# Optimization experiments

Hardware: AMD Instinct MI355X
Metric: run time of the kernel (lower is better)

## Reference

```python
import jax, jax.numpy as jnp
import numpy as np

B = 1_000_000
N_DIR, N_TRIAL = 2, 4
ALPHA, R_GAS, EPS = 0.3, 8.314462618, 1e-12
TAU_CLIP, LN_CLIP = 10.0, 20.0
EPS_FD, SIGMA, MARGIN = 1e-4, 0.05, 0.0
LAM_PHY, LAM_GD, LAM_TPD = 1.0, 0.1, 0.1


def renorm3(x):
    # clamp to >=0 and normalize so components sum to 1 (last axis)
    x = jnp.maximum(x, 0.0)
    return x / jnp.maximum(x.sum(-1, keepdims=True), EPS)


def nrtl_ln_gamma(x, T, g):
    # x: (B,3), T: (B,), g: (B,3,3) -> ln_gamma: (B,3)
    x = jnp.maximum(x, 0.0)
    Tc = jnp.maximum(T, 1.0)
    tau = jnp.clip(g / (R_GAS * jnp.maximum(Tc, EPS)[:, None, None]), -TAU_CLIP, TAU_CLIP)
    G = jnp.exp(-ALPHA * tau)
    denom = jnp.maximum(jnp.einsum('bj,bji->bi', x, G), EPS)          # (B,3)
    A = jnp.einsum('bj,bji->bi', x, tau * G)                          # (B,3), == num1 in torch
    term1 = A / denom
    W = x[:, None, :] * G / denom[:, None, :]                         # (B,3,3)
    inside = tau - (A / denom)[:, None, :]
    term2 = (W * inside).sum(-1)
    return jnp.clip(term1 + term2, -LN_CLIP, LN_CLIP)


def setup_inputs() -> dict:
    key = jax.random.key(0)
    k1, k2, k3, k4, k5, k6 = jax.random.split(key, 6)
    pred = jax.random.uniform(k1, (B, 6), dtype=jnp.float32, minval=0.01, maxval=1.0)
    target = jax.random.uniform(k2, (B, 6), dtype=jnp.float32, minval=0.01, maxval=1.0)
    T = 298.0 + 100.0 * jax.random.uniform(k3, (B,), dtype=jnp.float32)  # Kelvin
    g = 800.0 * jax.random.normal(k4, (B, 3, 3), dtype=jnp.float32)      # J/mol
    # simplex directions: zero-sum, unit-norm (matches _sample_simplex_directions)
    v = jax.random.normal(k5, (N_DIR, B, 3), dtype=jnp.float32)
    v = v - v.mean(-1, keepdims=True)
    dirs = v / jnp.maximum(jnp.linalg.norm(v, axis=-1, keepdims=True), 1e-12)
    noise = SIGMA * jax.random.normal(k6, (N_TRIAL, B, 3), dtype=jnp.float32)
    return {'pred': pred, 'target': target, 'T': T, 'g': g, 'dirs': dirs, 'noise': noise}


def reference(pred, target, T, g, dirs, noise):
    # supervised MSE on (E+R) compositions
    L_sup = jnp.mean((pred - target) ** 2)

    xE = renorm3(pred[:, :3])
    xR = renorm3(pred[:, 3:])
    ln_gE = nrtl_ln_gamma(xE, T, g)
    ln_gR = nrtl_ln_gamma(xR, T, g)
    # chemical potential residual r_k = ln(xE_k gE_k) - ln(xR_k gR_k)
    r = jnp.log(jnp.maximum(xE, EPS)) + ln_gE - (jnp.log(jnp.maximum(xR, EPS)) + ln_gR)
    L_phy = jnp.mean(r ** 2)

    lg = jax.vmap(lambda xx: nrtl_ln_gamma(xx, T, g))  # over trial/direction axis

    # Gibbs-Duhem finite-difference penalty along simplex directions
    x_p = renorm3(xE[None] + EPS_FD * dirs)            # (N_DIR,B,3)
    x_m = renorm3(xE[None] - EPS_FD * dirs)
    d_ln = (lg(x_p) - lg(x_m)) / (2.0 * EPS_FD)
    gd = (xE[None] * d_ln).sum(-1)                     # (N_DIR,B)
    L_gd = jnp.mean(gd * gd)

    # TPD stability penalty
    w = renorm3(xE[None] + noise)                      # (N_TRIAL,B,3)
    ln_gw = lg(w)
    tpd = (w * (jnp.log(jnp.maximum(w, EPS)) + ln_gw
                - jnp.log(jnp.maximum(xE, EPS))[None] - ln_gE[None])).sum(-1)
    L_tpd = jnp.mean(jnp.maximum(MARGIN - tpd, 0.0))

    return L_sup + LAM_PHY * L_phy + LAM_GD * L_gd + LAM_TPD * L_tpd
```

## Files before the change

### kernel.cpp

```cpp
#include <hip/hip_runtime.h>


constexpr float ALPHA   = 0.3f;
constexpr float R_GAS   = 8.314462618f;
constexpr float EPS     = 1e-12f;
constexpr float TAU_CLIP= 10.0f;
constexpr float LN_CLIP = 20.0f;
constexpr float EPS_FD  = 1e-4f;
constexpr float LAM_PHY = 1.0f;
constexpr float LAM_GD  = 0.1f;
constexpr float LAM_TPD = 0.1f;

__device__ __forceinline__ float clipf(float v, float lo, float hi) {
    return fminf(fmaxf(v, lo), hi);
}

struct Mats {
    float tau[3][3];
    float G[3][3];
    float tG[3][3];
};

__device__ __forceinline__ void ln_gamma3(const float x[3], const Mats& M, float lg[3]) {
    float ratio[3], invd[3];
#pragma unroll
    for (int i = 0; i < 3; ++i) {
        float d = x[0] * M.G[0][i] + x[1] * M.G[1][i] + x[2] * M.G[2][i];
        d = fmaxf(d, EPS);
        float A = x[0] * M.tG[0][i] + x[1] * M.tG[1][i] + x[2] * M.tG[2][i];
        float inv = 1.0f / d;
        invd[i] = inv;
        ratio[i] = A * inv;
    }
#pragma unroll
    for (int i = 0; i < 3; ++i) {
        float s = ratio[i];
#pragma unroll
        for (int j = 0; j < 3; ++j) {
            s += x[j] * M.G[i][j] * invd[j] * (M.tau[i][j] - ratio[j]);
        }
        lg[i] = clipf(s, -LN_CLIP, LN_CLIP);
    }
}

__device__ __forceinline__ void renorm3(float x[3]) {
    x[0] = fmaxf(x[0], 0.0f);
    x[1] = fmaxf(x[1], 0.0f);
    x[2] = fmaxf(x[2], 0.0f);
    float inv = 1.0f / fmaxf(x[0] + x[1] + x[2], EPS);
    x[0] *= inv; x[1] *= inv; x[2] *= inv;
}

__global__ __launch_bounds__(256) void nrtl_loss_kernel(
    const float* __restrict__ pred,
    const float* __restrict__ target,
    const float* __restrict__ Tarr,
    const float* __restrict__ g,
    const float* __restrict__ dirs,
    const float* __restrict__ noise,
    double* __restrict__ acc, int B)
{
    const int i = blockIdx.x * blockDim.x + threadIdx.x;
    float contrib = 0.0f;

    if (i < B) {
        float sup = 0.0f;
        float p6[6];
#pragma unroll
        for (int k = 0; k < 6; ++k) {
            float pv = pred[i * 6 + k];
            float tv = target[i * 6 + k];
            float d  = pv - tv;
            sup += d * d;
            p6[k] = pv;
        }

        float xE[3] = {p6[0], p6[1], p6[2]};
        float xR[3] = {p6[3], p6[4], p6[5]};
        renorm3(xE);
        renorm3(xR);

        const float Tc = fmaxf(Tarr[i], 1.0f);
        const float invRT = 1.0f / (R_GAS * Tc);
        Mats M;
#pragma unroll
        for (int a = 0; a < 3; ++a) {
#pragma unroll
            for (int b = 0; b < 3; ++b) {
                float ta = clipf(g[i * 9 + a * 3 + b] * invRT, -TAU_CLIP, TAU_CLIP);
                float Gv = expf(-ALPHA * ta);
                M.tau[a][b] = ta;
                M.G[a][b]   = Gv;
                M.tG[a][b]  = ta * Gv;
            }
        }

        float lgE[3], lgR[3];
        ln_gamma3(xE, M, lgE);
        ln_gamma3(xR, M, lgR);

        float logxE[3];
        float phy = 0.0f;
#pragma unroll
        for (int k = 0; k < 3; ++k) {
            logxE[k] = logf(fmaxf(xE[k], EPS));
            float r = logxE[k] + lgE[k] - logf(fmaxf(xR[k], EPS)) - lgR[k];
            phy += r * r;
        }

        float gdsum = 0.0f;
#pragma unroll
        for (int d = 0; d < 2; ++d) {
            float dv[3];
#pragma unroll
            for (int k = 0; k < 3; ++k) dv[k] = dirs[(d * B + i) * 3 + k];
            float xp[3], xm[3];
#pragma unroll
            for (int k = 0; k < 3; ++k) {
                xp[k] = xE[k] + EPS_FD * dv[k];
                xm[k] = xE[k] - EPS_FD * dv[k];
            }
            renorm3(xp);
            renorm3(xm);
            float lgp[3], lgm[3];
            ln_gamma3(xp, M, lgp);
            ln_gamma3(xm, M, lgm);
            float gd = 0.0f;
            const float inv2e = 0.5f / EPS_FD;
#pragma unroll
            for (int k = 0; k < 3; ++k) gd += xE[k] * ((lgp[k] - lgm[k]) * inv2e);
            gdsum += gd * gd;
        }

        float tpdsum = 0.0f;
#pragma unroll
        for (int t = 0; t < 4; ++t) {
            float w[3];
#pragma unroll
            for (int k = 0; k < 3; ++k) w[k] = xE[k] + noise[(t * B + i) * 3 + k];
            renorm3(w);
            float lgw[3];
            ln_gamma3(w, M, lgw);
            float tpd = 0.0f;
#pragma unroll
            for (int k = 0; k < 3; ++k) {
                tpd += w[k] * (logf(fmaxf(w[k], EPS)) + lgw[k] - logxE[k] - lgE[k]);
            }
            tpdsum += fmaxf(-tpd, 0.0f);
        }

        const float invB = 1.0f / (float)B;
        contrib = invB * (sup * (1.0f / 6.0f)
                          + LAM_PHY * phy * (1.0f / 3.0f)
                          + LAM_GD  * gdsum * 0.5f
                          + LAM_TPD * tpdsum * 0.25f);
    }

#pragma unroll
    for (int off = 32; off > 0; off >>= 1)
        contrib += __shfl_down(contrib, off, 64);

    __shared__ float ssum[4];
    const int lane = threadIdx.x & 63;
    const int wid  = threadIdx.x >> 6;
    if (lane == 0) ssum[wid] = contrib;
    __syncthreads();
    if (threadIdx.x == 0) {
        float bs = ssum[0] + ssum[1] + ssum[2] + ssum[3];
        atomicAdd(acc, (double)bs);
    }
}

__global__ void zero_ws_kernel(double* acc) { acc[0] = 0.0; }

__global__ void finalize_kernel(const double* acc, float* out) {
    out[0] = (float)acc[0];
}

extern "C" void kernel_launch(void* const* d_in, const int* in_sizes, int n_in,
                              void* d_out, int out_size, void* d_ws, size_t ws_size,
                              hipStream_t stream) {
    const float* pred   = (const float*)d_in[0];
    const float* target = (const float*)d_in[1];
    const float* Tarr   = (const float*)d_in[2];
    const float* g      = (const float*)d_in[3];
    const float* dirs   = (const float*)d_in[4];
    const float* noise  = (const float*)d_in[5];
    const int B = in_sizes[2];

    double* acc = (double*)d_ws;
    float*  out = (float*)d_out;

    zero_ws_kernel<<<1, 1, 0, stream>>>(acc);
    const int block = 256;
    const int grid  = (B + block - 1) / block;
    nrtl_loss_kernel<<<grid, block, 0, stream>>>(pred, target, Tarr, g, dirs, noise, acc, B);
    finalize_kernel<<<1, 1, 0, stream>>>(acc, out);
}
```

Measured before the change: 190.5 us.

## Use hardware rcp/exp2/log intrinsics, vectorize loads, replace atomics with partial reduction

Replaces IEEE divisions, expf and logf with AMD hardware approximate rcp, exp2 and log2 intrinsics to cut transcendental instruction cost. Loads pred and target as float2. Replaces the per-block double atomicAdd, plus its zero and finalize kernels, with per-block float partials summed by a single-block reduction kernel, removing atomic contention and one launch. The approximate intrinsics lose a few ulp of accuracy, and the finite-difference Gibbs-Duhem term may amplify that error.

```diff
diff --git a/kernel.cpp b/kernel.cpp
--- a/kernel.cpp
+++ b/kernel.cpp
@@ -1,19 +1,25 @@
 #include <hip/hip_runtime.h>
 
 
-constexpr float ALPHA   = 0.3f;
-constexpr float R_GAS   = 8.314462618f;
-constexpr float EPS     = 1e-12f;
-constexpr float TAU_CLIP= 10.0f;
-constexpr float LN_CLIP = 20.0f;
-constexpr float EPS_FD  = 1e-4f;
-constexpr float LAM_PHY = 1.0f;
-constexpr float LAM_GD  = 0.1f;
-constexpr float LAM_TPD = 0.1f;
+constexpr float ALPHA    = 0.3f;
+constexpr float R_GAS    = 8.314462618f;
+constexpr float EPS      = 1e-12f;
+constexpr float TAU_CLIP = 10.0f;
+constexpr float LN_CLIP  = 20.0f;
+constexpr float EPS_FD   = 1e-4f;
+constexpr float LAM_PHY  = 1.0f;
+constexpr float LAM_GD   = 0.1f;
+constexpr float LAM_TPD  = 0.1f;
+
+constexpr float LOG2E = 1.44269504088896340736f;
+constexpr float LN2   = 0.69314718055994530942f;
 
 __device__ __forceinline__ float clipf(float v, float lo, float hi) {
     return fminf(fmaxf(v, lo), hi);
 }
+__device__ __forceinline__ float fast_rcp(float x) { return __builtin_amdgcn_rcpf(x); }
+__device__ __forceinline__ float fast_exp(float x) { return __expf(x); }
+__device__ __forceinline__ float fast_log(float x) { return __logf(x); }
 
 struct Mats {
     float tau[3][3];
@@ -28,7 +34,7 @@
         float d = x[0] * M.G[0][i] + x[1] * M.G[1][i] + x[2] * M.G[2][i];
         d = fmaxf(d, EPS);
         float A = x[0] * M.tG[0][i] + x[1] * M.tG[1][i] + x[2] * M.tG[2][i];
-        float inv = 1.0f / d;
+        float inv = fast_rcp(d);
         invd[i] = inv;
         ratio[i] = A * inv;
     }
@@ -47,7 +53,7 @@
     x[0] = fmaxf(x[0], 0.0f);
     x[1] = fmaxf(x[1], 0.0f);
     x[2] = fmaxf(x[2], 0.0f);
-    float inv = 1.0f / fmaxf(x[0] + x[1] + x[2], EPS);
+    float inv = fast_rcp(fmaxf(x[0] + x[1] + x[2], EPS));
     x[0] *= inv; x[1] *= inv; x[2] *= inv;
 }
 
@@ -58,21 +64,24 @@
     const float* __restrict__ g,
     const float* __restrict__ dirs,
     const float* __restrict__ noise,
-    double* __restrict__ acc, int B)
+    float* __restrict__ partials, int B)
 {
     const int i = blockIdx.x * blockDim.x + threadIdx.x;
     float contrib = 0.0f;
 
     if (i < B) {
+        const float2* p2 = (const float2*)(pred   + i * 6);
+        const float2* t2 = (const float2*)(target + i * 6);
         float sup = 0.0f;
         float p6[6];
 #pragma unroll
-        for (int k = 0; k < 6; ++k) {
-            float pv = pred[i * 6 + k];
-            float tv = target[i * 6 + k];
-            float d  = pv - tv;
-            sup += d * d;
-            p6[k] = pv;
+        for (int k = 0; k < 3; ++k) {
+            float2 pv = p2[k];
+            float2 tv = t2[k];
+            float dx = pv.x - tv.x, dy = pv.y - tv.y;
+            sup += dx * dx + dy * dy;
+            p6[2 * k]     = pv.x;
+            p6[2 * k + 1] = pv.y;
         }
 
         float xE[3] = {p6[0], p6[1], p6[2]};
@@ -81,14 +90,14 @@
         renorm3(xR);
 
         const float Tc = fmaxf(Tarr[i], 1.0f);
-        const float invRT = 1.0f / (R_GAS * Tc);
+        const float invRT = fast_rcp(R_GAS * Tc);
         Mats M;
 #pragma unroll
         for (int a = 0; a < 3; ++a) {
 #pragma unroll
             for (int b = 0; b < 3; ++b) {
                 float ta = clipf(g[i * 9 + a * 3 + b] * invRT, -TAU_CLIP, TAU_CLIP);
-                float Gv = expf(-ALPHA * ta);
+                float Gv = __builtin_amdgcn_exp2f((-ALPHA * LOG2E) * ta);
                 M.tau[a][b] = ta;
                 M.G[a][b]   = Gv;
                 M.tG[a][b]  = ta * Gv;
@@ -103,8 +112,9 @@
         float phy = 0.0f;
 #pragma unroll
         for (int k = 0; k < 3; ++k) {
-            logxE[k] = logf(fmaxf(xE[k], EPS));
-            float r = logxE[k] + lgE[k] - logf(fmaxf(xR[k], EPS)) - lgR[k];
+            logxE[k] = LN2 * __builtin_amdgcn_logf(fmaxf(xE[k], EPS));
+            float logxR = LN2 * __builtin_amdgcn_logf(fmaxf(xR[k], EPS));
+            float r = logxE[k] + lgE[k] - logxR - lgR[k];
             phy += r * r;
         }
 
@@ -144,7 +154,8 @@
             float tpd = 0.0f;
 #pragma unroll
             for (int k = 0; k < 3; ++k) {
-                tpd += w[k] * (logf(fmaxf(w[k], EPS)) + lgw[k] - logxE[k] - lgE[k]);
+                float logw = LN2 * __builtin_amdgcn_logf(fmaxf(w[k], EPS));
+                tpd += w[k] * (logw + lgw[k] - logxE[k] - lgE[k]);
             }
             tpdsum += fmaxf(-tpd, 0.0f);
         }
@@ -166,15 +177,24 @@
     if (lane == 0) ssum[wid] = contrib;
     __syncthreads();
     if (threadIdx.x == 0) {
-        float bs = ssum[0] + ssum[1] + ssum[2] + ssum[3];
-        atomicAdd(acc, (double)bs);
-    }
-}
-
-__global__ void zero_ws_kernel(double* acc) { acc[0] = 0.0; }
-
-__global__ void finalize_kernel(const double* acc, float* out) {
-    out[0] = (float)acc[0];
+        partials[blockIdx.x] = ssum[0] + ssum[1] + ssum[2] + ssum[3];
+    }
+}
+
+__global__ __launch_bounds__(256) void reduce_kernel(
+    const float* __restrict__ partials, int n, float* __restrict__ out)
+{
+    double s = 0.0;
+    for (int j = threadIdx.x; j < n; j += 256) s += (double)partials[j];
+#pragma unroll
+    for (int off = 32; off > 0; off >>= 1)
+        s += __shfl_down(s, off, 64);
+    __shared__ double ds[4];
+    const int lane = threadIdx.x & 63;
+    const int wid  = threadIdx.x >> 6;
+    if (lane == 0) ds[wid] = s;
+    __syncthreads();
+    if (threadIdx.x == 0) out[0] = (float)(ds[0] + ds[1] + ds[2] + ds[3]);
 }
 
 extern "C" void kernel_launch(void* const* d_in, const int* in_sizes, int n_in,
@@ -188,12 +208,11 @@
     const float* noise  = (const float*)d_in[5];
     const int B = in_sizes[2];
 
-    double* acc = (double*)d_ws;
-    float*  out = (float*)d_out;
-
-    zero_ws_kernel<<<1, 1, 0, stream>>>(acc);
+    float* partials = (float*)d_ws;
+    float* out      = (float*)d_out;
+
     const int block = 256;
     const int grid  = (B + block - 1) / block;
-    nrtl_loss_kernel<<<grid, block, 0, stream>>>(pred, target, Tarr, g, dirs, noise, acc, B);
-    finalize_kernel<<<1, 1, 0, stream>>>(acc, out);
-}
+    nrtl_loss_kernel<<<grid, block, 0, stream>>>(pred, target, Tarr, g, dirs, noise, partials, B);
+    reduce_kernel<<<1, block, 0, stream>>>(partials, grid, out);
+}
```

After: 181.6 us. 4.7% less time.
